# Kernel tuning notes

Hardware: AMD Instinct MI355X
Metric: run time of the kernel (lower is better)

The kernel has to match this reference:

```python
import jax, jax.numpy as jnp
import numpy as np

B = 128        # graphs
N_PER = 1024   # nodes per graph
K = 7          # knn neighbors
X_SIZE = 16
POS_SIZE = 3
H1, H2 = 64, 128
N = B * N_PER
EPS = 1e-5


def _lin_init(key, din, dout):
    kw, kb = jax.random.split(key)
    s = 1.0 / np.sqrt(din)
    w = jax.random.uniform(kw, (din, dout), jnp.float32, -s, s)
    b = jax.random.uniform(kb, (dout,), jnp.float32, -s, s)
    return w, b


def setup_inputs() -> dict:
    key = jax.random.key(0)
    ks = jax.random.split(key, 12)
    x = jax.random.normal(ks[0], (N, X_SIZE), jnp.float32)
    pos = jax.random.normal(ks[1], (N, POS_SIZE), jnp.float32)
    batch = jnp.repeat(jnp.arange(B, dtype=jnp.int32), N_PER)
    wk1, bk1 = _lin_init(ks[2], X_SIZE, H1)
    wq1, bq1 = _lin_init(ks[3], X_SIZE, H1)
    wv1, bv1 = _lin_init(ks[4], X_SIZE, H1)
    ws1, bs1 = _lin_init(ks[5], X_SIZE, H1)
    wk2, bk2 = _lin_init(ks[6], H1, H2)
    wq2, bq2 = _lin_init(ks[7], H1, H2)
    wv2, bv2 = _lin_init(ks[8], H1, H2)
    ws2, bs2 = _lin_init(ks[9], H1, H2)
    g1 = jnp.ones((H1,), jnp.float32); be1 = jnp.zeros((H1,), jnp.float32)
    g2 = jnp.ones((H2,), jnp.float32); be2 = jnp.zeros((H2,), jnp.float32)
    return dict(x=x, pos=pos, batch=batch,
                wk1=wk1, bk1=bk1, wq1=wq1, bq1=bq1, wv1=wv1, bv1=bv1, ws1=ws1, bs1=bs1, g1=g1, be1=be1,
                wk2=wk2, bk2=bk2, wq2=wq2, bq2=bq2, wv2=wv2, bv2=bv2, ws2=ws2, bs2=bs2, g2=g2, be2=be2)


def knn_edges(pos):
    # batch-aware kNN: graphs are equal-sized contiguous blocks of N_PER nodes
    p = pos.reshape(B, N_PER, POS_SIZE)
    def per_graph(pg):
        d = jnp.sum((pg[:, None, :] - pg[None, :, :]) ** 2, axis=-1)  # [n, n]
        d = jnp.where(jnp.eye(N_PER, dtype=bool), jnp.inf, d)          # no self loops
        _, idx = jax.lax.top_k(-d, K)                                   # [n, K]
        return idx
    idx = jax.vmap(per_graph)(p)                       # [B, N_PER, K]
    offs = (jnp.arange(B) * N_PER)[:, None, None]
    src = (idx + offs).reshape(-1)                     # neighbor j (source)
    dst = jnp.broadcast_to(jnp.arange(N_PER)[None, :, None] + offs, (B, N_PER, K)).reshape(-1)
    return src, dst


def res_gated_conv(x, src, dst, wk, bk, wq, bq, wv, bv, ws, bs):
    # out_i = skip(x_i) + sum_{j->i} sigmoid(K x_i + Q x_j) * V x_j
    kf = x @ wk + bk
    qf = x @ wq + bq
    vf = x @ wv + bv
    msg = jax.nn.sigmoid(kf[dst] + qf[src]) * vf[src]  # [E, out]
    agg = jnp.zeros_like(kf).at[dst].add(msg)
    return agg + x @ ws + bs


def batch_norm(x, gamma, beta):
    m = x.mean(0)
    v = jnp.mean((x - m) ** 2, 0)  # biased var (training-mode BN)
    return (x - m) * jax.lax.rsqrt(v + EPS) * gamma + beta


def reference(x, pos, batch, wk1, bk1, wq1, bq1, wv1, bv1, ws1, bs1, g1, be1,
              wk2, bk2, wq2, bq2, wv2, bv2, ws2, bs2, g2, be2):
    src, dst = knn_edges(pos)
    h = jax.nn.relu(batch_norm(res_gated_conv(x, src, dst, wk1, bk1, wq1, bq1, wv1, bv1, ws1, bs1), g1, be1))
    h = jax.nn.relu(batch_norm(res_gated_conv(h, src, dst, wk2, bk2, wq2, bq2, wv2, bv2, ws2, bs2), g2, be2))
    s = jax.ops.segment_sum(h, batch, num_segments=B)
    cnt = jax.ops.segment_sum(jnp.ones((h.shape[0], 1), h.dtype), batch, num_segments=B)
    return s / cnt
```

## Files before the change

### kernel.cpp

```cpp
#include <hip/hip_runtime.h>
#include <hip/hip_bf16.h>

#define BGR   128
#define NPER  1024
#define NK    7
#define NNODES (BGR*NPER)

typedef __attribute__((ext_vector_type(8))) short short8;
typedef __attribute__((ext_vector_type(8))) unsigned short ushort8;
typedef __attribute__((ext_vector_type(4))) float floatx4;

static __device__ __forceinline__ float bf2f(unsigned short u) {
    unsigned int x = ((unsigned int)u) << 16;
    return __builtin_bit_cast(float, x);
}
static __device__ __forceinline__ unsigned short f2bf(float f) {
    unsigned int x = __builtin_bit_cast(unsigned int, f);
    unsigned int lsb = (x >> 16) & 1u;
    x += 0x7fffu + lsb;
    return (unsigned short)(x >> 16);
}
static __device__ __forceinline__ float packdi(float d, int j) {
    unsigned int ub = (__builtin_bit_cast(unsigned int, d) & 0xFFFFFC00u) | (unsigned int)j;
    return __builtin_bit_cast(float, ub);
}

__global__ __launch_bounds__(256) void knn_kernel(const float* __restrict__ pos,
                                                  int* __restrict__ idx) {
    __shared__ __align__(16) floatx4 sp[8 * 129];
    int g     = blockIdx.x >> 4;
    int qbase = (blockIdx.x & 15) << 6;
    int base  = g * NPER;
    const float* pg = pos + (size_t)base * 3;
    for (int t = threadIdx.x; t < NPER * 3; t += 256) {
        float v = pg[t];
        int j = t / 3, comp = t - j * 3;
        int slot = (j >> 7) * 129 + (j & 127);
        ((float*)&sp[slot])[comp] = v;
    }
    __syncthreads();
    for (int j = threadIdx.x; j < NPER; j += 256) {
        int slot = (j >> 7) * 129 + (j & 127);
        floatx4 q = sp[slot];
        sp[slot].w = fmaf(q.x, q.x, fmaf(q.y, q.y, q.z * q.z));
    }
    __syncthreads();

    int lane = threadIdx.x & 63;
    int wv   = (int)threadIdx.x >> 6;
    int grp  = lane >> 3;
    int e    = lane & 7;
    int qA_l = qbase + (wv * 8 + grp) * 2;
    int qB_l = qA_l + 1;
    floatx4 meA = sp[(qA_l >> 7) * 129 + (qA_l & 127)];
    floatx4 meB = sp[(qB_l >> 7) * 129 + (qB_l & 127)];
    float mAx = -2.f * meA.x, mAy = -2.f * meA.y, mAz = -2.f * meA.z;
    float mBx = -2.f * meB.x, mBy = -2.f * meB.y, mBz = -2.f * meB.z;
    const floatx4* cp = sp + e * 129;
    int jbase = e << 7;

    float a0=3e38f,a1=3e38f,a2=3e38f,a3=3e38f,a4=3e38f,a5=3e38f,a6=3e38f,a7=3e38f;
    float c0=3e38f,c1=3e38f,c2=3e38f,c3=3e38f,c4=3e38f,c5=3e38f,c6=3e38f,c7=3e38f;
    for (int jp = 0; jp < 128; jp += 4) {
        #pragma unroll
        for (int u = 0; u < 4; ++u) {
            floatx4 q = cp[jp + u];
            float dA = fmaf(mAx, q.x, fmaf(mAy, q.y, fmaf(mAz, q.z, q.w)));
            float dB = fmaf(mBx, q.x, fmaf(mBy, q.y, fmaf(mBz, q.z, q.w)));
            float tA = packdi(dA, jbase + jp + u);
            float tB = packdi(dB, jbase + jp + u);
            float nA7 = __builtin_amdgcn_fmed3f(a6, a7, tA);
            float nA6 = __builtin_amdgcn_fmed3f(a5, a6, tA);
            float nA5 = __builtin_amdgcn_fmed3f(a4, a5, tA);
            float nA4 = __builtin_amdgcn_fmed3f(a3, a4, tA);
            float nA3 = __builtin_amdgcn_fmed3f(a2, a3, tA);
            float nA2 = __builtin_amdgcn_fmed3f(a1, a2, tA);
            float nA1 = __builtin_amdgcn_fmed3f(a0, a1, tA);
            a0 = fminf(a0, tA);
            a1 = nA1; a2 = nA2; a3 = nA3; a4 = nA4; a5 = nA5; a6 = nA6; a7 = nA7;
            float nB7 = __builtin_amdgcn_fmed3f(c6, c7, tB);
            float nB6 = __builtin_amdgcn_fmed3f(c5, c6, tB);
            float nB5 = __builtin_amdgcn_fmed3f(c4, c5, tB);
            float nB4 = __builtin_amdgcn_fmed3f(c3, c4, tB);
            float nB3 = __builtin_amdgcn_fmed3f(c2, c3, tB);
            float nB2 = __builtin_amdgcn_fmed3f(c1, c2, tB);
            float nB1 = __builtin_amdgcn_fmed3f(c0, c1, tB);
            c0 = fminf(c0, tB);
            c1 = nB1; c2 = nB2; c3 = nB3; c4 = nB4; c5 = nB5; c6 = nB6; c7 = nB7;
        }
    }

    float A[8] = {a0,a1,a2,a3,a4,a5,a6,a7};
    float C[8] = {c0,c1,c2,c3,c4,c5,c6,c7};
    #pragma unroll
    for (int st = 0; st < 2; ++st) {
        int mask = 1 << st;
        #pragma unroll
        for (int ch = 0; ch < 2; ++ch) {
            float* L = ch ? C : A;
            float B[8], T[8];
            #pragma unroll
            for (int i = 0; i < 8; ++i) B[i] = __shfl_xor(L[i], mask);
            #pragma unroll
            for (int i = 0; i < 8; ++i) T[i] = fminf(L[i], B[7 - i]);
            #define CEx(x,y) { float mn = fminf(T[x], T[y]); float mx = fmaxf(T[x], T[y]); T[x] = mn; T[y] = mx; }
            CEx(0,4) CEx(1,5) CEx(2,6) CEx(3,7)
            CEx(0,2) CEx(1,3) CEx(4,6) CEx(5,7)
            CEx(0,1) CEx(2,3) CEx(4,5) CEx(6,7)
            #undef CEx
            #pragma unroll
            for (int i = 0; i < 8; ++i) L[i] = T[i];
        }
    }
    float OA[8], OC[8];
    #pragma unroll
    for (int i = 0; i < 8; ++i) { OA[i] = __shfl_xor(A[i], 4); OC[i] = __shfl_xor(C[i], 4); }

    if (e < 2) {
        float *M, *O;
        int qm_l;
        if (e == 0) { M = A;  O = OA; qm_l = qA_l; }
        else        { M = C;  O = OC; qm_l = qB_l; }
        bool selfInM = (qm_l >> 9) == 0;
        int r[7];
        #pragma unroll
        for (int i = 0; i < 7; ++i) {
            float mm = selfInM ? fminf(M[i + 1], O[6 - i]) : fminf(O[i + 1], M[6 - i]);
            r[i] = base + (int)(__builtin_bit_cast(unsigned int, mm) & 1023u);
        }
        int4* op = (int4*)(idx + (size_t)(base + qm_l) * 8);
        int4 r0, r1;
        r0.x = r[0]; r0.y = r[1]; r0.z = r[2]; r0.w = r[3];
        r1.x = r[4]; r1.y = r[5]; r1.z = r[6]; r1.w = base;
        op[0] = r0;
        op[1] = r1;
    }
}

__global__ __launch_bounds__(256) void feat1_kernel(
    const float* __restrict__ x,
    const float* __restrict__ wk, const float* __restrict__ bk,
    const float* __restrict__ wq, const float* __restrict__ bq,
    const float* __restrict__ wv, const float* __restrict__ bv,
    const float* __restrict__ wsm, const float* __restrict__ bs,
    unsigned int* __restrict__ qv, unsigned int* __restrict__ ks) {
    __shared__ unsigned short xh[2][2][16][17];
    int m  = threadIdx.x >> 6;
    int l  = threadIdx.x & 63;
    int lr = l & 15;
    int gq = l >> 4;
    const float* wm  = (m == 0) ? wk : (m == 1) ? wq : (m == 2) ? wv : wsm;
    const float* bmp = (m == 0) ? bk : (m == 1) ? bq : (m == 2) ? bv : bs;
    short8 W[4];
    #pragma unroll
    for (int ct = 0; ct < 4; ++ct) {
        short8 w;
        #pragma unroll
        for (int e = 0; e < 8; ++e) {
            int k = gq * 8 + e;
            float v = (gq < 2) ? wm[(size_t)k * 64 + ct * 16 + lr] : 0.f;
            w[e] = (short)f2bf(v);
        }
        W[ct] = w;
    }
    float bvv[4];
    #pragma unroll
    for (int ct = 0; ct < 4; ++ct) bvv[ct] = bmp[ct * 16 + lr];

    for (int t = 0; t < 8; ++t) {
        int nt = blockIdx.x * 8 + t;
        int n  = nt * 16 + lr;
        short8 a;
        if (gq < 2) {
            const floatx4* xr = (const floatx4*)(x + (size_t)n * 16 + gq * 8);
            floatx4 v0 = xr[0], v1 = xr[1];
            a[0] = (short)f2bf(v0.x); a[1] = (short)f2bf(v0.y);
            a[2] = (short)f2bf(v0.z); a[3] = (short)f2bf(v0.w);
            a[4] = (short)f2bf(v1.x); a[5] = (short)f2bf(v1.y);
            a[6] = (short)f2bf(v1.z); a[7] = (short)f2bf(v1.w);
        } else {
            #pragma unroll
            for (int e = 0; e < 8; ++e) a[e] = 0;
        }
        #pragma unroll
        for (int ct = 0; ct < 4; ++ct) {
            float bv = bvv[ct];
            floatx4 acc = {bv, bv, bv, bv};
            acc = __builtin_amdgcn_mfma_f32_16x16x32_bf16(a, W[ct], acc, 0, 0, 0);
            if (m >= 2) {
                #pragma unroll
                for (int r = 0; r < 4; ++r)
                    xh[ct & 1][m - 2][gq * 4 + r][lr] = f2bf(acc[r]);
            }
            __syncthreads();
            if (m < 2) {
                unsigned int* od = (m == 1) ? qv : ks;
                int set = (m == 1) ? 0 : 1;
                #pragma unroll
                for (int r = 0; r < 4; ++r) {
                    unsigned int lo = f2bf(acc[r]);
                    unsigned int hi = xh[ct & 1][set][gq * 4 + r][lr];
                    od[(size_t)(nt * 16 + gq * 4 + r) * 64 + ct * 16 + lr] = (hi << 16) | lo;
                }
            }
        }
    }
}

__global__ __launch_bounds__(256) void conv64_kernel(
    const unsigned int* __restrict__ qv, const unsigned int* __restrict__ ks,
    const int* __restrict__ idx, unsigned short* __restrict__ h,
    float* __restrict__ part) {
    int c   = threadIdx.x & 63;
    int sub = __builtin_amdgcn_readfirstlane((int)(threadIdx.x >> 6));
    int b     = blockIdx.x;
    int xcd   = b & 7;
    int chunk = b >> 3;
    int graph = xcd * 16 + (chunk >> 5);
    int nblk  = chunk & 31;
    int n0 = graph * NPER + nblk * 32;
    float s = 0.f, s2 = 0.f;
    #pragma unroll 8
    for (int i = sub; i < 32; i += 4) {
        int n = n0 + i;
        const int4* nb4 = (const int4*)(idx + (size_t)n * 8);
        int4 na = nb4[0];
        int4 nbv = nb4[1];
        unsigned int ku = ks[(size_t)n * 64 + c];
        float kv  = bf2f((unsigned short)(ku & 0xFFFF));
        float acc = bf2f((unsigned short)(ku >> 16));
        int jj[7] = {na.x, na.y, na.z, na.w, nbv.x, nbv.y, nbv.z};
        #pragma unroll
        for (int k = 0; k < NK; ++k) {
            int j = __builtin_amdgcn_readfirstlane(jj[k]);
            unsigned int u = qv[(size_t)j * 64 + c];
            float qvv = bf2f((unsigned short)(u & 0xFFFF));
            float vvv = bf2f((unsigned short)(u >> 16));
            float t = kv + qvv;
            float sg = __builtin_amdgcn_rcpf(1.f + __expf(-t));
            acc = fmaf(sg, vvv, acc);
        }
        unsigned short hb = f2bf(acc);
        h[(size_t)n * 64 + c] = hb;
        float hv = bf2f(hb);
        s += hv; s2 += hv * hv;
    }
    __shared__ float ls[256], ls2[256];
    ls[threadIdx.x] = s; ls2[threadIdx.x] = s2;
    __syncthreads();
    if (threadIdx.x < 64) {
        #pragma unroll
        for (int l = 1; l < 4; ++l) { s += ls[threadIdx.x + l*64]; s2 += ls2[threadIdx.x + l*64]; }
        part[(size_t)blockIdx.x * 128 + threadIdx.x]      = s;
        part[(size_t)blockIdx.x * 128 + 64 + threadIdx.x] = s2;
    }
}

__global__ __launch_bounds__(256) void conv128_kernel(
    const unsigned int* __restrict__ qv, const unsigned int* __restrict__ ks,
    const int* __restrict__ idx, unsigned int* __restrict__ h,
    float* __restrict__ part) {
    int lane = threadIdx.x & 63;
    int w    = __builtin_amdgcn_readfirstlane((int)(threadIdx.x >> 6));
    int b     = blockIdx.x;
    int xcd   = b & 7;
    int chunk = b >> 3;
    int graph = xcd * 16 + (chunk >> 5);
    int nblk  = chunk & 31;
    int n0 = graph * NPER + nblk * 32;
    float s0 = 0.f, s1 = 0.f, q0s = 0.f, q1s = 0.f;
    #pragma unroll 4
    for (int i = w; i < 32; i += 4) {
        int n = n0 + i;
        const int4* nb4 = (const int4*)(idx + (size_t)n * 8);
        int4 na = nb4[0];
        int4 nbv = nb4[1];
        const uint2* krow = (const uint2*)(ks + (size_t)n * 128);
        uint2 ku = krow[lane];
        float kv0  = bf2f((unsigned short)(ku.x & 0xFFFF));
        float acc0 = bf2f((unsigned short)(ku.x >> 16));
        float kv1  = bf2f((unsigned short)(ku.y & 0xFFFF));
        float acc1 = bf2f((unsigned short)(ku.y >> 16));
        int jj[7] = {na.x, na.y, na.z, na.w, nbv.x, nbv.y, nbv.z};
        #pragma unroll
        for (int k = 0; k < NK; ++k) {
            int j = __builtin_amdgcn_readfirstlane(jj[k]);
            const uint2* p = (const uint2*)(qv + (size_t)j * 128);
            uint2 u = p[lane];
            float qa = bf2f((unsigned short)(u.x & 0xFFFF));
            float va = bf2f((unsigned short)(u.x >> 16));
            float qb = bf2f((unsigned short)(u.y & 0xFFFF));
            float vb = bf2f((unsigned short)(u.y >> 16));
            float sga = __builtin_amdgcn_rcpf(1.f + __expf(-(kv0 + qa)));
            float sgb = __builtin_amdgcn_rcpf(1.f + __expf(-(kv1 + qb)));
            acc0 = fmaf(sga, va, acc0);
            acc1 = fmaf(sgb, vb, acc1);
        }
        unsigned int hb0 = f2bf(acc0);
        unsigned int hb1 = f2bf(acc1);
        h[(size_t)n * 64 + lane] = (hb1 << 16) | hb0;
        float hv0 = bf2f((unsigned short)hb0);
        float hv1 = bf2f((unsigned short)hb1);
        s0 += hv0; q0s += hv0 * hv0;
        s1 += hv1; q1s += hv1 * hv1;
    }
    __shared__ float r0[256], r1[256], r2[256], r3[256];
    r0[threadIdx.x] = s0; r1[threadIdx.x] = s1; r2[threadIdx.x] = q0s; r3[threadIdx.x] = q1s;
    __syncthreads();
    if (threadIdx.x < 64) {
        #pragma unroll
        for (int k = 1; k < 4; ++k) {
            s0  += r0[threadIdx.x + 64 * k]; s1  += r1[threadIdx.x + 64 * k];
            q0s += r2[threadIdx.x + 64 * k]; q1s += r3[threadIdx.x + 64 * k];
        }
        float* pr = part + (size_t)blockIdx.x * 256;
        pr[2 * threadIdx.x]           = s0;
        pr[2 * threadIdx.x + 1]       = s1;
        pr[128 + 2 * threadIdx.x]     = q0s;
        pr[128 + 2 * threadIdx.x + 1] = q1s;
    }
}

template<int C>
static __device__ __forceinline__ void bnfin_body(
    const float* __restrict__ part, const float* __restrict__ gamma,
    const float* __restrict__ beta, float* __restrict__ ss,
    int c, float* ls, float* ls2) {
    float s = 0.f, s2 = 0.f;
    for (int b = threadIdx.x; b < 4096; b += 256) {
        s  += part[(size_t)b * 2 * C + c];
        s2 += part[(size_t)b * 2 * C + C + c];
    }
    ls[threadIdx.x] = s; ls2[threadIdx.x] = s2;
    __syncthreads();
    for (int st = 128; st > 0; st >>= 1) {
        if (threadIdx.x < st) { ls[threadIdx.x] += ls[threadIdx.x+st]; ls2[threadIdx.x] += ls2[threadIdx.x+st]; }
        __syncthreads();
    }
    if (threadIdx.x == 0) {
        float m   = ls[0] / (float)NNODES;
        float var = ls2[0] / (float)NNODES - m * m;
        float inv = rsqrtf(var + 1e-5f);
        float sc  = gamma[c] * inv;
        ss[c]     = sc;
        ss[C + c] = beta[c] - m * sc;
    }
}

template<int C>
__global__ __launch_bounds__(256) void bnfin_kernel(
    const float* __restrict__ part, const float* __restrict__ gamma,
    const float* __restrict__ beta, float* __restrict__ ss) {
    __shared__ float ls[256], ls2[256];
    bnfin_body<C>(part, gamma, beta, ss, blockIdx.x, ls, ls2);
}

__global__ __launch_bounds__(256) void fin1_wfrag_kernel(
    const float* __restrict__ part, const float* __restrict__ gamma,
    const float* __restrict__ beta, float* __restrict__ ss,
    const float* __restrict__ w0, const float* __restrict__ w1,
    const float* __restrict__ w2, const float* __restrict__ w3,
    unsigned short* __restrict__ frag) {
    __shared__ float ls[256], ls2[256];
    if (blockIdx.x < 64) {
        bnfin_body<64>(part, gamma, beta, ss, blockIdx.x, ls, ls2);
        return;
    }
    int s  = blockIdx.x - 64;
    if (threadIdx.x >= 64) return;
    int m  = s >> 4;
    int kt = (s >> 3) & 1;
    int ct = s & 7;
    const float* w = (m == 0) ? w0 : (m == 1) ? w1 : (m == 2) ? w2 : w3;
    int l = threadIdx.x;
    int col = ct * 16 + (l & 15);
    int kbase = kt * 32 + (l >> 4) * 8;
    unsigned short* out = frag + ((size_t)s * 64 + l) * 8;
    #pragma unroll
    for (int e = 0; e < 8; ++e) out[e] = f2bf(w[(size_t)(kbase + e) * 128 + col]);
}

__global__ __launch_bounds__(256) void feat2_kernel(
    const unsigned short* __restrict__ h1n, const unsigned short* __restrict__ frag,
    const float* __restrict__ ss1,
    const float* __restrict__ b0, const float* __restrict__ b1,
    const float* __restrict__ b2, const float* __restrict__ b3,
    unsigned int* __restrict__ qv2, unsigned int* __restrict__ ks2) {
    __shared__ unsigned short xh[2][2][16][17];
    int m  = threadIdx.x >> 6;
    int l  = threadIdx.x & 63;
    const float* bm = (m == 0) ? b0 : (m == 1) ? b1 : (m == 2) ? b2 : b3;
    int lr = l & 15;
    int gq = l >> 4;
    short8 W0[8], W1[8];
    #pragma unroll
    for (int ct = 0; ct < 8; ++ct) {
        W0[ct] = *(const short8*)(frag + ((size_t)(m * 16 + ct)     * 64 + l) * 8);
        W1[ct] = *(const short8*)(frag + ((size_t)(m * 16 + 8 + ct) * 64 + l) * 8);
    }
    float bvv[8];
    #pragma unroll
    for (int ct = 0; ct < 8; ++ct) bvv[ct] = bm[ct * 16 + lr];

    for (int t = 0; t < 8; ++t) {
        int nt = blockIdx.x * 8 + t;
        int n  = nt * 16 + lr;
        const unsigned short* ar = h1n + (size_t)n * 64 + gq * 8;
        short8 a0r = *(const short8*)ar;
        short8 a1r = *(const short8*)(ar + 32);
        short8 a0, a1;
        #pragma unroll
        for (int e = 0; e < 8; ++e) {
            int c0 = gq * 8 + e;
            float f0 = bf2f((unsigned short)a0r[e]) * ss1[c0] + ss1[64 + c0];
            a0[e] = (short)f2bf(fmaxf(f0, 0.f));
            int c1 = 32 + gq * 8 + e;
            float f1 = bf2f((unsigned short)a1r[e]) * ss1[c1] + ss1[64 + c1];
            a1[e] = (short)f2bf(fmaxf(f1, 0.f));
        }
        #pragma unroll
        for (int ct = 0; ct < 8; ++ct) {
            float bv = bvv[ct];
            floatx4 acc = {bv, bv, bv, bv};
            acc = __builtin_amdgcn_mfma_f32_16x16x32_bf16(a0, W0[ct], acc, 0, 0, 0);
            acc = __builtin_amdgcn_mfma_f32_16x16x32_bf16(a1, W1[ct], acc, 0, 0, 0);
            if (m >= 2) {
                #pragma unroll
                for (int r = 0; r < 4; ++r)
                    xh[ct & 1][m - 2][gq * 4 + r][lr] = f2bf(acc[r]);
            }
            __syncthreads();
            if (m < 2) {
                unsigned int* od = (m == 1) ? qv2 : ks2;
                int set = (m == 1) ? 0 : 1;
                #pragma unroll
                for (int r = 0; r < 4; ++r) {
                    unsigned int lo = f2bf(acc[r]);
                    unsigned int hi = xh[ct & 1][set][gq * 4 + r][lr];
                    od[(size_t)(nt * 16 + gq * 4 + r) * 128 + ct * 16 + lr] = (hi << 16) | lo;
                }
            }
        }
    }
}

__global__ __launch_bounds__(256) void pool_partial_kernel(const unsigned int* __restrict__ h2p,
                                                           const float* __restrict__ ss2,
                                                           float* __restrict__ part) {
    int g = blockIdx.x >> 3;
    int q = blockIdx.x & 7;
    int cp = (threadIdx.x & 63) * 2;
    int isub = threadIdx.x >> 6;
    float sc0 = ss2[cp],     sh0 = ss2[128 + cp];
    float sc1 = ss2[cp + 1], sh1 = ss2[128 + cp + 1];
    float acc0 = 0.f, acc1 = 0.f;
    const unsigned int* hp = h2p + ((size_t)g * NPER + q * 128) * 64 + (cp >> 1);
    for (int i = isub; i < 128; i += 4) {
        unsigned int u = hp[(size_t)i * 64];
        acc0 += fmaxf(bf2f((unsigned short)(u & 0xFFFF)) * sc0 + sh0, 0.f);
        acc1 += fmaxf(bf2f((unsigned short)(u >> 16))    * sc1 + sh1, 0.f);
    }
    __shared__ float red0[256], red1[256];
    red0[threadIdx.x] = acc0; red1[threadIdx.x] = acc1;
    __syncthreads();
    if (threadIdx.x < 64) {
        float s0 = acc0, s1 = acc1;
        #pragma unroll
        for (int k = 1; k < 4; ++k) { s0 += red0[threadIdx.x + 64 * k]; s1 += red1[threadIdx.x + 64 * k]; }
        part[(size_t)blockIdx.x * 128 + cp]     = s0;
        part[(size_t)blockIdx.x * 128 + cp + 1] = s1;
    }
}

__global__ void pool_final_kernel(const float* __restrict__ part, float* __restrict__ out) {
    int g = blockIdx.x, c = threadIdx.x;
    float s = 0.f;
    #pragma unroll
    for (int q = 0; q < 8; ++q) s += part[(size_t)(g * 8 + q) * 128 + c];
    out[(size_t)g * 128 + c] = s * (1.f / 1024.f);
}

extern "C" void kernel_launch(void* const* d_in, const int* in_sizes, int n_in,
                              void* d_out, int out_size, void* d_ws, size_t ws_size,
                              hipStream_t stream) {
    const float* x   = (const float*)d_in[0];
    const float* pos = (const float*)d_in[1];
    const float* wk1 = (const float*)d_in[3];
    const float* bk1 = (const float*)d_in[4];
    const float* wq1 = (const float*)d_in[5];
    const float* bq1 = (const float*)d_in[6];
    const float* wv1 = (const float*)d_in[7];
    const float* bv1 = (const float*)d_in[8];
    const float* ws1 = (const float*)d_in[9];
    const float* bs1 = (const float*)d_in[10];
    const float* g1  = (const float*)d_in[11];
    const float* be1 = (const float*)d_in[12];
    const float* wk2 = (const float*)d_in[13];
    const float* bk2 = (const float*)d_in[14];
    const float* wq2 = (const float*)d_in[15];
    const float* bq2 = (const float*)d_in[16];
    const float* wv2 = (const float*)d_in[17];
    const float* bv2 = (const float*)d_in[18];
    const float* ws2 = (const float*)d_in[19];
    const float* bs2 = (const float*)d_in[20];
    const float* g2  = (const float*)d_in[21];
    const float* be2 = (const float*)d_in[22];
    float* out = (float*)d_out;

    const size_t SZ_QV1 = (size_t)NNODES * 64 * 4;
    const size_t SZ_QV2 = (size_t)NNODES * 128 * 4;

    char* ws = (char*)d_ws;
    size_t off = 0;
    auto alloc = [&](size_t b) { size_t o = off; off += (b + 255) & ~(size_t)255; return o; };

    int* idx              = (int*)(ws + alloc((size_t)NNODES * 8 * 4));
    size_t o_region       = alloc(2 * SZ_QV2);
    unsigned int* qv1     = (unsigned int*)(ws + o_region);
    unsigned int* ks1     = (unsigned int*)(ws + o_region + SZ_QV1);
    unsigned int* qv2     = (unsigned int*)(ws + o_region);
    unsigned int* ks2     = (unsigned int*)(ws + o_region + SZ_QV2);
    unsigned short* h1    = (unsigned short*)(ws + alloc((size_t)NNODES * 64 * 2));
    unsigned int* h2      = (unsigned int*)(ws + alloc((size_t)NNODES * 64 * 4));
    unsigned short* frag  = (unsigned short*)(ws + alloc(64 * 64 * 8 * 2));
    float* part           = (float*)(ws + alloc((size_t)4096 * 2 * 128 * 4));
    float* ss1            = (float*)(ws + alloc(2 * 64 * 4));
    float* ss2            = (float*)(ws + alloc(2 * 128 * 4));
    (void)ws_size; (void)in_sizes; (void)n_in; (void)out_size;

    knn_kernel<<<BGR * 16, 256, 0, stream>>>(pos, idx);
    feat1_kernel<<<NNODES / 128, 256, 0, stream>>>(x, wk1, bk1, wq1, bq1, wv1, bv1, ws1, bs1,
                                                   qv1, ks1);
    conv64_kernel<<<NNODES / 32, 256, 0, stream>>>(qv1, ks1, idx, h1, part);
    fin1_wfrag_kernel<<<128, 256, 0, stream>>>(part, g1, be1, ss1,
                                               wk2, wq2, wv2, ws2, frag);
    feat2_kernel<<<NNODES / 128, 256, 0, stream>>>(h1, frag, ss1, bk2, bq2, bv2, bs2,
                                                   qv2, ks2);
    conv128_kernel<<<NNODES / 32, 256, 0, stream>>>(qv2, ks2, idx, h2, part);
    bnfin_kernel<128><<<128, 256, 0, stream>>>(part, g2, be2, ss2);
    pool_partial_kernel<<<BGR * 8, 256, 0, stream>>>(h2, ss2, part);
    pool_final_kernel<<<BGR, 128, 0, stream>>>(part, out);
}
```

Baseline: 219.9 us.

## Fuse BN finalize and pooling into one kernel with grid-wide atomic sync

Replaces the three tail kernels (BN2 statistics finalize, pool partial, pool final) with one 1024-block kernel. The first 256 blocks reduce BN partials in parallel, block 0 computes the scale/shift and publishes it through an atomic flag, and the other blocks spin-wait before pooling. The last block per graph, found with an atomic counter, writes the final mean. This removes two kernel launches and their gaps, but depends on every spinning block being co-resident and adds spin-wait latency. Sync counters are reset inside fin1_wfrag_kernel.

```diff
diff --git a/kernel.cpp b/kernel.cpp
--- a/kernel.cpp
+++ b/kernel.cpp
@@ -347,21 +347,15 @@
     }
 }
 
-template<int C>
-__global__ __launch_bounds__(256) void bnfin_kernel(
-    const float* __restrict__ part, const float* __restrict__ gamma,
-    const float* __restrict__ beta, float* __restrict__ ss) {
-    __shared__ float ls[256], ls2[256];
-    bnfin_body<C>(part, gamma, beta, ss, blockIdx.x, ls, ls2);
-}
-
 __global__ __launch_bounds__(256) void fin1_wfrag_kernel(
     const float* __restrict__ part, const float* __restrict__ gamma,
     const float* __restrict__ beta, float* __restrict__ ss,
     const float* __restrict__ w0, const float* __restrict__ w1,
     const float* __restrict__ w2, const float* __restrict__ w3,
-    unsigned short* __restrict__ frag) {
+    unsigned short* __restrict__ frag, unsigned int* __restrict__ syncb) {
     __shared__ float ls[256], ls2[256];
+    if (blockIdx.x == 127 && threadIdx.x >= 64 && threadIdx.x < 194)
+        syncb[threadIdx.x - 64] = 0u;
     if (blockIdx.x < 64) {
         bnfin_body<64>(part, gamma, beta, ss, blockIdx.x, ls, ls2);
         return;
@@ -444,13 +438,60 @@
     }
 }
 
-__global__ __launch_bounds__(256) void pool_partial_kernel(const unsigned int* __restrict__ h2p,
-                                                           const float* __restrict__ ss2,
-                                                           float* __restrict__ part) {
-    int g = blockIdx.x >> 3;
-    int q = blockIdx.x & 7;
-    int cp = (threadIdx.x & 63) * 2;
-    int isub = threadIdx.x >> 6;
+__global__ __launch_bounds__(256, 4) void bn_pool_kernel(
+    const float* __restrict__ part, const float* __restrict__ gamma,
+    const float* __restrict__ beta, const unsigned int* __restrict__ h2p,
+    float* __restrict__ part2, float* __restrict__ ss2,
+    float* __restrict__ pool_part, unsigned int* __restrict__ syncb,
+    float* __restrict__ out) {
+    int b = blockIdx.x;
+    int t = threadIdx.x;
+    if (b < 256) {
+        float s = 0.f;
+        #pragma unroll 4
+        for (int r = 0; r < 16; ++r)
+            s += part[(size_t)(b * 16 + r) * 256 + t];
+        part2[(size_t)b * 256 + t] = s;
+        __threadfence();
+        __syncthreads();
+        if (t == 0)
+            __hip_atomic_fetch_add(&syncb[0], 1u, __ATOMIC_RELEASE, __HIP_MEMORY_SCOPE_AGENT);
+    }
+    if (b == 0) {
+        if (t == 0) {
+            while (__hip_atomic_load(&syncb[0], __ATOMIC_ACQUIRE, __HIP_MEMORY_SCOPE_AGENT) < 256u)
+                __builtin_amdgcn_s_sleep(2);
+        }
+        __syncthreads();
+        __threadfence();
+        float acc = 0.f;
+        for (int bb = 0; bb < 256; ++bb) acc += part2[(size_t)bb * 256 + t];
+        __shared__ float sums[256];
+        sums[t] = acc;
+        __syncthreads();
+        if (t < 128) {
+            float m   = sums[t] * (1.f / (float)NNODES);
+            float var = sums[128 + t] * (1.f / (float)NNODES) - m * m;
+            float inv = rsqrtf(var + 1e-5f);
+            float sc  = gamma[t] * inv;
+            ss2[t]       = sc;
+            ss2[128 + t] = beta[t] - m * sc;
+        }
+        __threadfence();
+        __syncthreads();
+        if (t == 0)
+            __hip_atomic_store(&syncb[1], 1u, __ATOMIC_RELEASE, __HIP_MEMORY_SCOPE_AGENT);
+    } else {
+        if (t == 0) {
+            while (__hip_atomic_load(&syncb[1], __ATOMIC_ACQUIRE, __HIP_MEMORY_SCOPE_AGENT) == 0u)
+                __builtin_amdgcn_s_sleep(2);
+        }
+        __syncthreads();
+        __threadfence();
+    }
+    int g = b >> 3, q = b & 7;
+    int cp = (t & 63) * 2;
+    int isub = t >> 6;
     float sc0 = ss2[cp],     sh0 = ss2[128 + cp];
     float sc1 = ss2[cp + 1], sh1 = ss2[128 + cp + 1];
     float acc0 = 0.f, acc1 = 0.f;
@@ -461,23 +502,30 @@
         acc1 += fmaxf(bf2f((unsigned short)(u >> 16))    * sc1 + sh1, 0.f);
     }
     __shared__ float red0[256], red1[256];
-    red0[threadIdx.x] = acc0; red1[threadIdx.x] = acc1;
-    __syncthreads();
-    if (threadIdx.x < 64) {
+    red0[t] = acc0; red1[t] = acc1;
+    __syncthreads();
+    if (t < 64) {
         float s0 = acc0, s1 = acc1;
         #pragma unroll
-        for (int k = 1; k < 4; ++k) { s0 += red0[threadIdx.x + 64 * k]; s1 += red1[threadIdx.x + 64 * k]; }
-        part[(size_t)blockIdx.x * 128 + cp]     = s0;
-        part[(size_t)blockIdx.x * 128 + cp + 1] = s1;
-    }
-}
-
-__global__ void pool_final_kernel(const float* __restrict__ part, float* __restrict__ out) {
-    int g = blockIdx.x, c = threadIdx.x;
-    float s = 0.f;
-    #pragma unroll
-    for (int q = 0; q < 8; ++q) s += part[(size_t)(g * 8 + q) * 128 + c];
-    out[(size_t)g * 128 + c] = s * (1.f / 1024.f);
+        for (int k = 1; k < 4; ++k) { s0 += red0[t + 64 * k]; s1 += red1[t + 64 * k]; }
+        pool_part[(size_t)b * 128 + cp]     = s0;
+        pool_part[(size_t)b * 128 + cp + 1] = s1;
+    }
+    __threadfence();
+    __syncthreads();
+    __shared__ unsigned int oldsh;
+    if (t == 0)
+        oldsh = __hip_atomic_fetch_add(&syncb[2 + g], 1u, __ATOMIC_ACQ_REL, __HIP_MEMORY_SCOPE_AGENT);
+    __syncthreads();
+    if (oldsh == 7u) {
+        __threadfence();
+        if (t < 128) {
+            float ssum = 0.f;
+            #pragma unroll
+            for (int qq = 0; qq < 8; ++qq) ssum += pool_part[(size_t)(g * 8 + qq) * 128 + t];
+            out[(size_t)g * 128 + t] = ssum * (1.f / 1024.f);
+        }
+    }
 }
 
 extern "C" void kernel_launch(void* const* d_in, const int* in_sizes, int n_in,
@@ -524,8 +572,11 @@
     unsigned int* h2      = (unsigned int*)(ws + alloc((size_t)NNODES * 64 * 4));
     unsigned short* frag  = (unsigned short*)(ws + alloc(64 * 64 * 8 * 2));
     float* part           = (float*)(ws + alloc((size_t)4096 * 2 * 128 * 4));
+    float* part2          = (float*)(ws + alloc((size_t)256 * 256 * 4));
+    float* pool_part      = (float*)(ws + alloc((size_t)1024 * 128 * 4));
     float* ss1            = (float*)(ws + alloc(2 * 64 * 4));
     float* ss2            = (float*)(ws + alloc(2 * 128 * 4));
+    unsigned int* syncb   = (unsigned int*)(ws + alloc(130 * 4));
     (void)ws_size; (void)in_sizes; (void)n_in; (void)out_size;
 
     knn_kernel<<<BGR * 16, 256, 0, stream>>>(pos, idx);
@@ -533,11 +584,10 @@
                                                    qv1, ks1);
     conv64_kernel<<<NNODES / 32, 256, 0, stream>>>(qv1, ks1, idx, h1, part);
     fin1_wfrag_kernel<<<128, 256, 0, stream>>>(part, g1, be1, ss1,
-                                               wk2, wq2, wv2, ws2, frag);
+                                               wk2, wq2, wv2, ws2, frag, syncb);
     feat2_kernel<<<NNODES / 128, 256, 0, stream>>>(h1, frag, ss1, bk2, bq2, bv2, bs2,
                                                    qv2, ks2);
     conv128_kernel<<<NNODES / 32, 256, 0, stream>>>(qv2, ks2, idx, h2, part);
-    bnfin_kernel<128><<<128, 256, 0, stream>>>(part, g2, be2, ss2);
-    pool_partial_kernel<<<BGR * 8, 256, 0, stream>>>(h2, ss2, part);
-    pool_final_kernel<<<BGR, 128, 0, stream>>>(part, out);
-}
+    bn_pool_kernel<<<1024, 256, 0, stream>>>(part, g2, be2, h2, part2, ss2,
+                                             pool_part, syncb, out);
+}
```

Result: slower. 568.0 us (+158.3%).
